# Performance work log

Measured on AMD Instinct MI355X. Metric: run time of the kernel, lower is better.

The kernel has to match this reference:

```python
import jax, jax.numpy as jnp
import numpy as np
from jax import lax

BETA = 0.5
ITERATIONS = 20
EPS = 1e-12


def setup_inputs() -> dict:
    key = jax.random.key(0)
    n, K = 32768, 512
    # C plays the role of a cosine-similarity matrix; randn keeps exp(C/beta) bounded.
    C = jax.random.normal(key, (n, K), dtype=jnp.float32)
    return {"C": C}


def reference(C):
    n, K = C.shape
    a = jnp.float32(1.0 / n)          # uniform row marginal (scalar broadcast of a = ones(n,1)/n)
    b = jnp.float32(1.0 / K)          # uniform column marginal
    K_mat = jnp.exp(C / BETA)         # [n, K]
    Q0 = jnp.full((n, K), 1.0 / (n * K), dtype=C.dtype)
    sigma0 = jnp.full((K,), 1.0 / K, dtype=C.dtype)

    def step(carry, _):
        Q, sigma = carry
        Q = K_mat * sigma[None, :]                              # elementwise column scaling
        Q = Q / (jnp.sum(Q, axis=1, keepdims=True) + EPS) * a   # row-normalize to marginal a
        sigma = b / (jnp.sum(Q, axis=0) + EPS)                  # column sums (== Q^T @ ones)
        return (Q, sigma), None

    (Q, sigma), _ = lax.scan(step, (Q0, sigma0), None, length=ITERATIONS)
    return Q * n
```

## Files before the change

### kernel.cpp

```cpp
#include <hip/hip_runtime.h>
#include <cmath>


namespace {
constexpr int ROWS = 32768;
constexpr int COLS = 512;
constexpr int ITERS = 20;
constexpr float EPS = 1e-12f;
constexpr float A_M = 1.0f / 32768.0f;
constexpr float B_M = 1.0f / 512.0f;
constexpr float L2E2 = 2.8853900817779268f;
constexpr int WPB = 4;
constexpr int NSH = 8;
constexpr int SLAB_ROWS = ROWS / 8;
constexpr int GSIG_OFF = 0;
constexpr int TSUM_OFF = ITERS * COLS;
constexpr int MID_BLOCKS = 1024;
constexpr int MID_RPW = 8;
constexpr int BIG_BLOCKS = 2048;
constexpr int BIG_RPW = 4;

typedef float f4v __attribute__((ext_vector_type(4)));
}

__device__ __forceinline__ float bflo(unsigned u) {
  union { unsigned i; float f; } v; v.i = u << 16; return v.f;
}
__device__ __forceinline__ float bfhi(unsigned u) {
  union { unsigned i; float f; } v; v.i = u & 0xFFFF0000u; return v.f;
}
__device__ __forceinline__ unsigned f2bf(float f) {
  union { float f; unsigned u; } v; v.f = f;
  return (v.u + 0x7FFFu + ((v.u >> 16) & 1u)) >> 16;
}
__device__ __forceinline__ int row_base_mid(int bid, int wave) {
  return (bid & 7) * SLAB_ROWS + ((bid >> 3) * WPB + wave) * MID_RPW;
}
__device__ __forceinline__ int row_base_big(int bid, int wave) {
  return (bid & 7) * SLAB_ROWS + ((bid >> 3) * WPB + wave) * BIG_RPW;
}

__global__ __launch_bounds__(256) void ipot_zero_kernel(float* __restrict__ ws) {
  const size_t stride = (size_t)gridDim.x * blockDim.x;
  const size_t gtid = (size_t)blockIdx.x * blockDim.x + threadIdx.x;
  if (gtid < COLS) ws[GSIG_OFF + gtid] = B_M;
  const size_t tsz = (size_t)(ITERS - 1) * NSH * COLS;
  for (size_t i = gtid; i < tsz; i += stride) ws[TSUM_OFF + i] = 0.0f;
}

__global__ __launch_bounds__(256, 8) void ipot_pass0_kernel(
    const float* __restrict__ C, float* __restrict__ out,
    float* __restrict__ ws) {
  __shared__ float part[WPB][COLS];
  const int tid = threadIdx.x;
  const int wave = tid >> 6;
  const int lane = tid & 63;
  const int wrow = row_base_big(blockIdx.x, wave);
  unsigned short* Kb = (unsigned short*)(out + (size_t)ROWS * COLS / 2);

  f4v c0[BIG_RPW], c1[BIG_RPW];
#pragma unroll
  for (int r = 0; r < BIG_RPW; ++r) {
    const f4v* rp = (const f4v*)(C + (size_t)(wrow + r) * COLS);
    c0[r] = rp[2 * lane];
    c1[r] = rp[2 * lane + 1];
  }

  float p[BIG_RPW];
#pragma unroll
  for (int r = 0; r < BIG_RPW; ++r) {
    c0[r].x = exp2f(c0[r].x * L2E2); c0[r].y = exp2f(c0[r].y * L2E2);
    c0[r].z = exp2f(c0[r].z * L2E2); c0[r].w = exp2f(c0[r].w * L2E2);
    c1[r].x = exp2f(c1[r].x * L2E2); c1[r].y = exp2f(c1[r].y * L2E2);
    c1[r].z = exp2f(c1[r].z * L2E2); c1[r].w = exp2f(c1[r].w * L2E2);
    uint4 kp;
    kp.x = f2bf(c0[r].x) | (f2bf(c0[r].y) << 16);
    kp.y = f2bf(c0[r].z) | (f2bf(c0[r].w) << 16);
    kp.z = f2bf(c1[r].x) | (f2bf(c1[r].y) << 16);
    kp.w = f2bf(c1[r].z) | (f2bf(c1[r].w) << 16);
    ((uint4*)(Kb + (size_t)(wrow + r) * COLS))[lane] = kp;
    p[r] = ((c0[r].x + c0[r].y) + (c0[r].z + c0[r].w)) +
           ((c1[r].x + c1[r].y) + (c1[r].z + c1[r].w));
  }
#pragma unroll
  for (int off = 32; off; off >>= 1) {
#pragma unroll
    for (int r = 0; r < BIG_RPW; ++r) p[r] += __shfl_xor(p[r], off, 64);
  }
  float a[8] = {0.f, 0.f, 0.f, 0.f, 0.f, 0.f, 0.f, 0.f};
#pragma unroll
  for (int r = 0; r < BIG_RPW; ++r) {
    const float inv = 1.0f / (B_M * p[r] + EPS);
    a[0] += c0[r].x * inv; a[1] += c0[r].y * inv;
    a[2] += c0[r].z * inv; a[3] += c0[r].w * inv;
    a[4] += c1[r].x * inv; a[5] += c1[r].y * inv;
    a[6] += c1[r].z * inv; a[7] += c1[r].w * inv;
  }
  *(float4*)&part[wave][8 * lane] = *(float4*)&a[0];
  *(float4*)&part[wave][8 * lane + 4] = *(float4*)&a[4];
  __syncthreads();
  float* ts = ws + TSUM_OFF + (size_t)(blockIdx.x & 7) * COLS;
  int j = tid;
  atomicAdd(&ts[j], part[0][j] + part[1][j] + part[2][j] + part[3][j]);
  j += 256;
  atomicAdd(&ts[j], part[0][j] + part[1][j] + part[2][j] + part[3][j]);
}

__global__ __launch_bounds__(256, 4) void ipot_mid_kernel(
    const float* __restrict__ base, float* __restrict__ ws, int t) {
  __shared__ float sig[COLS];
  __shared__ float part[WPB][COLS];
  const int tid = threadIdx.x;
  const int wave = tid >> 6;
  const int lane = tid & 63;
  const int wrow = row_base_mid(blockIdx.x, wave);
  const unsigned short* Kb =
      (const unsigned short*)(base + (size_t)ROWS * COLS / 2);

  const float* gsp = ws + GSIG_OFF + (size_t)(t - 1) * COLS;
  const float* tb = ws + TSUM_OFF + (size_t)(t - 1) * NSH * COLS;
  float tv0[NSH], tv1[NSH];
#pragma unroll
  for (int s = 0; s < NSH; ++s) {
    tv0[s] = tb[s * COLS + tid];
    tv1[s] = tb[s * COLS + tid + 256];
  }
  const float g0 = gsp[tid];
  const float g1 = gsp[tid + 256];

  uint4 kr[MID_RPW];
#pragma unroll
  for (int r = 0; r < MID_RPW; ++r)
    kr[r] = ((const uint4*)(Kb + (size_t)(wrow + r) * COLS))[lane];

  {
    float T0 = 0.f, T1 = 0.f;
#pragma unroll
    for (int s = 0; s < NSH; ++s) { T0 += tv0[s]; T1 += tv1[s]; }
    const float sv0 = B_M / (g0 * A_M * T0 + EPS);
    const float sv1 = B_M / (g1 * A_M * T1 + EPS);
    sig[tid] = sv0;
    sig[tid + 256] = sv1;
    if (blockIdx.x == 0) {
      float* gsc = ws + GSIG_OFF + (size_t)t * COLS;
      gsc[tid] = sv0;
      gsc[tid + 256] = sv1;
    }
  }
  __syncthreads();

  const float4 sA = *(const float4*)&sig[8 * lane];
  const float4 sB = *(const float4*)&sig[8 * lane + 4];

  float p[MID_RPW];
#pragma unroll
  for (int r = 0; r < MID_RPW; ++r) {
    p[r] = bflo(kr[r].x) * sA.x + bfhi(kr[r].x) * sA.y +
           bflo(kr[r].y) * sA.z + bfhi(kr[r].y) * sA.w +
           bflo(kr[r].z) * sB.x + bfhi(kr[r].z) * sB.y +
           bflo(kr[r].w) * sB.z + bfhi(kr[r].w) * sB.w;
  }
#pragma unroll
  for (int off = 32; off; off >>= 1) {
#pragma unroll
    for (int r = 0; r < MID_RPW; ++r) p[r] += __shfl_xor(p[r], off, 64);
  }
  float a[8] = {0.f, 0.f, 0.f, 0.f, 0.f, 0.f, 0.f, 0.f};
#pragma unroll
  for (int r = 0; r < MID_RPW; ++r) {
    const float inv = 1.0f / (p[r] + EPS);
    a[0] += bflo(kr[r].x) * inv; a[1] += bfhi(kr[r].x) * inv;
    a[2] += bflo(kr[r].y) * inv; a[3] += bfhi(kr[r].y) * inv;
    a[4] += bflo(kr[r].z) * inv; a[5] += bfhi(kr[r].z) * inv;
    a[6] += bflo(kr[r].w) * inv; a[7] += bfhi(kr[r].w) * inv;
  }
  *(float4*)&part[wave][8 * lane] = *(float4*)&a[0];
  *(float4*)&part[wave][8 * lane + 4] = *(float4*)&a[4];
  __syncthreads();
  float* ts = ws + TSUM_OFF +
              ((size_t)t * NSH + (blockIdx.x & 7)) * COLS;
  int j = tid;
  atomicAdd(&ts[j], part[0][j] + part[1][j] + part[2][j] + part[3][j]);
  j += 256;
  atomicAdd(&ts[j], part[0][j] + part[1][j] + part[2][j] + part[3][j]);
}

__global__ __launch_bounds__(256, 8) void ipot_final_kernel(
    const float* __restrict__ C, float* __restrict__ out,
    const float* __restrict__ ws) {
  __shared__ float sig[COLS];
  const int tid = threadIdx.x;
  const int wave = tid >> 6;
  const int lane = tid & 63;
  const int wrow = row_base_big(blockIdx.x, wave);

  const int t = ITERS - 1;
  const float* gsp = ws + GSIG_OFF + (size_t)(t - 1) * COLS;
  const float* tb = ws + TSUM_OFF + (size_t)(t - 1) * NSH * COLS;
  float tv0[NSH], tv1[NSH];
#pragma unroll
  for (int s = 0; s < NSH; ++s) {
    tv0[s] = tb[s * COLS + tid];
    tv1[s] = tb[s * COLS + tid + 256];
  }
  const float g0 = gsp[tid];
  const float g1 = gsp[tid + 256];

  f4v c0[BIG_RPW], c1[BIG_RPW];
#pragma unroll
  for (int r = 0; r < BIG_RPW; ++r) {
    const f4v* rp = (const f4v*)(C + (size_t)(wrow + r) * COLS);
    c0[r] = rp[2 * lane];
    c1[r] = rp[2 * lane + 1];
  }

  {
    float T0 = 0.f, T1 = 0.f;
#pragma unroll
    for (int s = 0; s < NSH; ++s) { T0 += tv0[s]; T1 += tv1[s]; }
    sig[tid] = B_M / (g0 * A_M * T0 + EPS);
    sig[tid + 256] = B_M / (g1 * A_M * T1 + EPS);
  }
  __syncthreads();

  const float4 sA = *(const float4*)&sig[8 * lane];
  const float4 sB = *(const float4*)&sig[8 * lane + 4];

  float p[BIG_RPW];
#pragma unroll
  for (int r = 0; r < BIG_RPW; ++r) {
    c0[r].x = exp2f(c0[r].x * L2E2); c0[r].y = exp2f(c0[r].y * L2E2);
    c0[r].z = exp2f(c0[r].z * L2E2); c0[r].w = exp2f(c0[r].w * L2E2);
    c1[r].x = exp2f(c1[r].x * L2E2); c1[r].y = exp2f(c1[r].y * L2E2);
    c1[r].z = exp2f(c1[r].z * L2E2); c1[r].w = exp2f(c1[r].w * L2E2);
    p[r] = c0[r].x * sA.x + c0[r].y * sA.y + c0[r].z * sA.z + c0[r].w * sA.w +
           c1[r].x * sB.x + c1[r].y * sB.y + c1[r].z * sB.z + c1[r].w * sB.w;
  }
#pragma unroll
  for (int off = 32; off; off >>= 1) {
#pragma unroll
    for (int r = 0; r < BIG_RPW; ++r) p[r] += __shfl_xor(p[r], off, 64);
  }
#pragma unroll
  for (int r = 0; r < BIG_RPW; ++r) {
    const float inv = 1.0f / (p[r] + EPS);
    f4v* wp = (f4v*)(out + (size_t)(wrow + r) * COLS);
    f4v o0, o1;
    o0.x = c0[r].x * sA.x * inv; o0.y = c0[r].y * sA.y * inv;
    o0.z = c0[r].z * sA.z * inv; o0.w = c0[r].w * sA.w * inv;
    o1.x = c1[r].x * sB.x * inv; o1.y = c1[r].y * sB.y * inv;
    o1.z = c1[r].z * sB.z * inv; o1.w = c1[r].w * sB.w * inv;
    __builtin_nontemporal_store(o0, &wp[2 * lane]);
    __builtin_nontemporal_store(o1, &wp[2 * lane + 1]);
  }
}

extern "C" void kernel_launch(void* const* d_in, const int* in_sizes, int n_in,
                              void* d_out, int out_size, void* d_ws, size_t ws_size,
                              hipStream_t stream) {
  const float* C = (const float*)d_in[0];
  float* out = (float*)d_out;
  float* ws = (float*)d_ws;

  ipot_zero_kernel<<<128, 256, 0, stream>>>(ws);
  ipot_pass0_kernel<<<BIG_BLOCKS, 256, 0, stream>>>(C, out, ws);
  for (int t = 1; t < ITERS - 1; ++t)
    ipot_mid_kernel<<<MID_BLOCKS, 256, 0, stream>>>(out, ws, t);
  ipot_final_kernel<<<BIG_BLOCKS, 256, 0, stream>>>(C, out, ws);
}
```

Before: 179.0 us.

## Keep bf16 kernel in workspace and compute final pass from it

When the workspace is large enough, the bf16 copy of exp(C/beta) now lives in the workspace instead of the second half of the output buffer. That frees the final kernel to read the 32 MB bf16 matrix rather than re-reading the 64 MB fp32 C and recomputing exp. Pass 0 also uses nontemporal loads for C in this mode. The final output is then built from bf16-rounded K values, which costs some precision, and the new path depends on the workspace size given by the harness.

```diff
diff --git a/kernel.cpp b/kernel.cpp
--- a/kernel.cpp
+++ b/kernel.cpp
@@ -15,6 +15,8 @@
 constexpr int SLAB_ROWS = ROWS / 8;
 constexpr int GSIG_OFF = 0;
 constexpr int TSUM_OFF = ITERS * COLS;
+constexpr size_t CTRL_FLOATS = (size_t)TSUM_OFF + (size_t)(ITERS - 1) * NSH * COLS;
+constexpr size_t KB_BYTES = (size_t)ROWS * COLS * 2;
 constexpr int MID_BLOCKS = 1024;
 constexpr int MID_RPW = 8;
 constexpr int BIG_BLOCKS = 2048;
@@ -40,30 +42,35 @@
   return (bid & 7) * SLAB_ROWS + ((bid >> 3) * WPB + wave) * BIG_RPW;
 }
 
-__global__ __launch_bounds__(256) void ipot_zero_kernel(float* __restrict__ ws) {
+__global__ __launch_bounds__(256) void ipot_zero_kernel(float* __restrict__ ctrl) {
   const size_t stride = (size_t)gridDim.x * blockDim.x;
   const size_t gtid = (size_t)blockIdx.x * blockDim.x + threadIdx.x;
-  if (gtid < COLS) ws[GSIG_OFF + gtid] = B_M;
+  if (gtid < COLS) ctrl[GSIG_OFF + gtid] = B_M;
   const size_t tsz = (size_t)(ITERS - 1) * NSH * COLS;
-  for (size_t i = gtid; i < tsz; i += stride) ws[TSUM_OFF + i] = 0.0f;
-}
-
+  for (size_t i = gtid; i < tsz; i += stride) ctrl[TSUM_OFF + i] = 0.0f;
+}
+
+template <bool NT_C>
 __global__ __launch_bounds__(256, 8) void ipot_pass0_kernel(
-    const float* __restrict__ C, float* __restrict__ out,
-    float* __restrict__ ws) {
+    const float* __restrict__ C, unsigned short* __restrict__ Kb,
+    float* __restrict__ ctrl) {
   __shared__ float part[WPB][COLS];
   const int tid = threadIdx.x;
   const int wave = tid >> 6;
   const int lane = tid & 63;
   const int wrow = row_base_big(blockIdx.x, wave);
-  unsigned short* Kb = (unsigned short*)(out + (size_t)ROWS * COLS / 2);
 
   f4v c0[BIG_RPW], c1[BIG_RPW];
 #pragma unroll
   for (int r = 0; r < BIG_RPW; ++r) {
     const f4v* rp = (const f4v*)(C + (size_t)(wrow + r) * COLS);
-    c0[r] = rp[2 * lane];
-    c1[r] = rp[2 * lane + 1];
+    if (NT_C) {
+      c0[r] = __builtin_nontemporal_load(&rp[2 * lane]);
+      c1[r] = __builtin_nontemporal_load(&rp[2 * lane + 1]);
+    } else {
+      c0[r] = rp[2 * lane];
+      c1[r] = rp[2 * lane + 1];
+    }
   }
 
   float p[BIG_RPW];
@@ -99,7 +106,7 @@
   *(float4*)&part[wave][8 * lane] = *(float4*)&a[0];
   *(float4*)&part[wave][8 * lane + 4] = *(float4*)&a[4];
   __syncthreads();
-  float* ts = ws + TSUM_OFF + (size_t)(blockIdx.x & 7) * COLS;
+  float* ts = ctrl + TSUM_OFF + (size_t)(blockIdx.x & 7) * COLS;
   int j = tid;
   atomicAdd(&ts[j], part[0][j] + part[1][j] + part[2][j] + part[3][j]);
   j += 256;
@@ -107,18 +114,16 @@
 }
 
 __global__ __launch_bounds__(256, 4) void ipot_mid_kernel(
-    const float* __restrict__ base, float* __restrict__ ws, int t) {
+    const unsigned short* __restrict__ Kb, float* __restrict__ ctrl, int t) {
   __shared__ float sig[COLS];
   __shared__ float part[WPB][COLS];
   const int tid = threadIdx.x;
   const int wave = tid >> 6;
   const int lane = tid & 63;
   const int wrow = row_base_mid(blockIdx.x, wave);
-  const unsigned short* Kb =
-      (const unsigned short*)(base + (size_t)ROWS * COLS / 2);
-
-  const float* gsp = ws + GSIG_OFF + (size_t)(t - 1) * COLS;
-  const float* tb = ws + TSUM_OFF + (size_t)(t - 1) * NSH * COLS;
+
+  const float* gsp = ctrl + GSIG_OFF + (size_t)(t - 1) * COLS;
+  const float* tb = ctrl + TSUM_OFF + (size_t)(t - 1) * NSH * COLS;
   float tv0[NSH], tv1[NSH];
 #pragma unroll
   for (int s = 0; s < NSH; ++s) {
@@ -142,7 +147,7 @@
     sig[tid] = sv0;
     sig[tid + 256] = sv1;
     if (blockIdx.x == 0) {
-      float* gsc = ws + GSIG_OFF + (size_t)t * COLS;
+      float* gsc = ctrl + GSIG_OFF + (size_t)t * COLS;
       gsc[tid] = sv0;
       gsc[tid + 256] = sv1;
     }
@@ -177,7 +182,7 @@
   *(float4*)&part[wave][8 * lane] = *(float4*)&a[0];
   *(float4*)&part[wave][8 * lane + 4] = *(float4*)&a[4];
   __syncthreads();
-  float* ts = ws + TSUM_OFF +
+  float* ts = ctrl + TSUM_OFF +
               ((size_t)t * NSH + (blockIdx.x & 7)) * COLS;
   int j = tid;
   atomicAdd(&ts[j], part[0][j] + part[1][j] + part[2][j] + part[3][j]);
@@ -185,9 +190,9 @@
   atomicAdd(&ts[j], part[0][j] + part[1][j] + part[2][j] + part[3][j]);
 }
 
-__global__ __launch_bounds__(256, 8) void ipot_final_kernel(
-    const float* __restrict__ C, float* __restrict__ out,
-    const float* __restrict__ ws) {
+__global__ __launch_bounds__(256, 8) void ipot_final_kb_kernel(
+    const unsigned short* __restrict__ Kb, float* __restrict__ out,
+    const float* __restrict__ ctrl) {
   __shared__ float sig[COLS];
   const int tid = threadIdx.x;
   const int wave = tid >> 6;
@@ -195,8 +200,8 @@
   const int wrow = row_base_big(blockIdx.x, wave);
 
   const int t = ITERS - 1;
-  const float* gsp = ws + GSIG_OFF + (size_t)(t - 1) * COLS;
-  const float* tb = ws + TSUM_OFF + (size_t)(t - 1) * NSH * COLS;
+  const float* gsp = ctrl + GSIG_OFF + (size_t)(t - 1) * COLS;
+  const float* tb = ctrl + TSUM_OFF + (size_t)(t - 1) * NSH * COLS;
   float tv0[NSH], tv1[NSH];
 #pragma unroll
   for (int s = 0; s < NSH; ++s) {
@@ -206,6 +211,71 @@
   const float g0 = gsp[tid];
   const float g1 = gsp[tid + 256];
 
+  uint4 kr[BIG_RPW];
+#pragma unroll
+  for (int r = 0; r < BIG_RPW; ++r)
+    kr[r] = ((const uint4*)(Kb + (size_t)(wrow + r) * COLS))[lane];
+
+  {
+    float T0 = 0.f, T1 = 0.f;
+#pragma unroll
+    for (int s = 0; s < NSH; ++s) { T0 += tv0[s]; T1 += tv1[s]; }
+    sig[tid] = B_M / (g0 * A_M * T0 + EPS);
+    sig[tid + 256] = B_M / (g1 * A_M * T1 + EPS);
+  }
+  __syncthreads();
+
+  const float4 sA = *(const float4*)&sig[8 * lane];
+  const float4 sB = *(const float4*)&sig[8 * lane + 4];
+
+  float p[BIG_RPW];
+#pragma unroll
+  for (int r = 0; r < BIG_RPW; ++r) {
+    p[r] = bflo(kr[r].x) * sA.x + bfhi(kr[r].x) * sA.y +
+           bflo(kr[r].y) * sA.z + bfhi(kr[r].y) * sA.w +
+           bflo(kr[r].z) * sB.x + bfhi(kr[r].z) * sB.y +
+           bflo(kr[r].w) * sB.z + bfhi(kr[r].w) * sB.w;
+  }
+#pragma unroll
+  for (int off = 32; off; off >>= 1) {
+#pragma unroll
+    for (int r = 0; r < BIG_RPW; ++r) p[r] += __shfl_xor(p[r], off, 64);
+  }
+#pragma unroll
+  for (int r = 0; r < BIG_RPW; ++r) {
+    const float inv = 1.0f / (p[r] + EPS);
+    f4v* wp = (f4v*)(out + (size_t)(wrow + r) * COLS);
+    f4v o0, o1;
+    o0.x = bflo(kr[r].x) * sA.x * inv; o0.y = bfhi(kr[r].x) * sA.y * inv;
+    o0.z = bflo(kr[r].y) * sA.z * inv; o0.w = bfhi(kr[r].y) * sA.w * inv;
+    o1.x = bflo(kr[r].z) * sB.x * inv; o1.y = bfhi(kr[r].z) * sB.y * inv;
+    o1.z = bflo(kr[r].w) * sB.z * inv; o1.w = bfhi(kr[r].w) * sB.w * inv;
+    __builtin_nontemporal_store(o0, &wp[2 * lane]);
+    __builtin_nontemporal_store(o1, &wp[2 * lane + 1]);
+  }
+}
+
+__global__ __launch_bounds__(256, 8) void ipot_final_c_kernel(
+    const float* __restrict__ C, float* __restrict__ out,
+    const float* __restrict__ ctrl) {
+  __shared__ float sig[COLS];
+  const int tid = threadIdx.x;
+  const int wave = tid >> 6;
+  const int lane = tid & 63;
+  const int wrow = row_base_big(blockIdx.x, wave);
+
+  const int t = ITERS - 1;
+  const float* gsp = ctrl + GSIG_OFF + (size_t)(t - 1) * COLS;
+  const float* tb = ctrl + TSUM_OFF + (size_t)(t - 1) * NSH * COLS;
+  float tv0[NSH], tv1[NSH];
+#pragma unroll
+  for (int s = 0; s < NSH; ++s) {
+    tv0[s] = tb[s * COLS + tid];
+    tv1[s] = tb[s * COLS + tid + 256];
+  }
+  const float g0 = gsp[tid];
+  const float g1 = gsp[tid + 256];
+
   f4v c0[BIG_RPW], c1[BIG_RPW];
 #pragma unroll
   for (int r = 0; r < BIG_RPW; ++r) {
@@ -213,7 +283,6 @@
     c0[r] = rp[2 * lane];
     c1[r] = rp[2 * lane + 1];
   }
-
   {
     float T0 = 0.f, T1 = 0.f;
 #pragma unroll
@@ -260,11 +329,27 @@
                               hipStream_t stream) {
   const float* C = (const float*)d_in[0];
   float* out = (float*)d_out;
-  float* ws = (float*)d_ws;
-
-  ipot_zero_kernel<<<128, 256, 0, stream>>>(ws);
-  ipot_pass0_kernel<<<BIG_BLOCKS, 256, 0, stream>>>(C, out, ws);
+
+  const bool kb_in_ws = ws_size >= KB_BYTES + CTRL_FLOATS * sizeof(float);
+  unsigned short* Kb;
+  float* ctrl;
+  if (kb_in_ws) {
+    Kb = (unsigned short*)d_ws;
+    ctrl = (float*)((char*)d_ws + KB_BYTES);
+  } else {
+    Kb = (unsigned short*)(out + (size_t)ROWS * COLS / 2);
+    ctrl = (float*)d_ws;
+  }
+
+  ipot_zero_kernel<<<128, 256, 0, stream>>>(ctrl);
+  if (kb_in_ws)
+    ipot_pass0_kernel<true><<<BIG_BLOCKS, 256, 0, stream>>>(C, Kb, ctrl);
+  else
+    ipot_pass0_kernel<false><<<BIG_BLOCKS, 256, 0, stream>>>(C, Kb, ctrl);
   for (int t = 1; t < ITERS - 1; ++t)
-    ipot_mid_kernel<<<MID_BLOCKS, 256, 0, stream>>>(out, ws, t);
-  ipot_final_kernel<<<BIG_BLOCKS, 256, 0, stream>>>(C, out, ws);
-}
+    ipot_mid_kernel<<<MID_BLOCKS, 256, 0, stream>>>(Kb, ctrl, t);
+  if (kb_in_ws)
+    ipot_final_kb_kernel<<<BIG_BLOCKS, 256, 0, stream>>>(Kb, out, ctrl);
+  else
+    ipot_final_c_kernel<<<BIG_BLOCKS, 256, 0, stream>>>(C, out, ctrl);
+}
```

Measured after the change: 185.0 us. 1.03x slower.
